# Kernel tuning notes

Hardware: AMD Instinct MI355X
Metric: run time of the kernel (lower is better)

The kernel has to match this reference:

```python
import jax, jax.numpy as jnp
import numpy as np

B, D, R, E, L = 16384, 1024, 64, 4, 2


def setup_inputs() -> dict:
    key = jax.random.key(0)
    ks = jax.random.split(key, 5)
    sU = (2.0 / (D + R)) ** 0.5  # glorot_normal std
    sC = (2.0 / (R + R)) ** 0.5
    sG = (2.0 / (D + 1)) ** 0.5
    return {
        "x": jax.random.normal(ks[0], (B, D), jnp.float32),
        "U": jax.random.normal(ks[1], (L, E, D, R), jnp.float32) * sU,
        "V": jax.random.normal(ks[2], (L, E, D, R), jnp.float32) * sU,
        "C": jax.random.normal(ks[3], (L, E, R, R), jnp.float32) * sC,
        "bias": jnp.zeros((L, D), jnp.float32),
        "gateW": jax.random.normal(ks[4], (E, D), jnp.float32) * sG,
    }


def reference(x, U, V, C, bias, gateW):
    # DCN-V2 mixture-of-low-rank-experts cross network.
    # x: [B, D]; U/V: [L, E, D, R]; C: [L, E, R, R]; bias: [L, D]; gateW: [E, D]
    x0 = x
    x_l = x
    for i in range(L):
        # gating: per-expert Dense(1, no bias) on current x_l -> softmax over experts
        gate = jax.nn.softmax(jnp.einsum('bd,ed->be', x_l, gateW), axis=-1)  # [B, E]
        # low-rank bilinear: U tanh(C tanh(V^T x)) , vectorized over experts
        v_x = jnp.tanh(jnp.einsum('edr,bd->ber', V[i], x_l))      # [B, E, R]
        c_x = jnp.tanh(jnp.einsum('erq,beq->ber', C[i], v_x))     # [B, E, R]
        uv_x = jnp.einsum('edr,ber->bed', U[i], c_x)              # [B, E, D]
        dot = x0[:, None, :] * (uv_x + bias[i][None, None, :])    # [B, E, D]
        moe_out = jnp.einsum('bed,be->bd', dot, gate)             # [B, D]
        x_l = moe_out + x_l  # residual (dropout_rate=0 -> identity)
    return x_l
```

## Files before the change

kernel.cpp:

```cpp
#include <hip/hip_runtime.h>
#include <stdint.h>


typedef __attribute__((ext_vector_type(8))) short bf16x8;
typedef __attribute__((ext_vector_type(4))) float f32x4;

#define MFMA_BF16(a, b, c) __builtin_amdgcn_mfma_f32_16x16x32_bf16((a), (b), (c), 0, 0, 0)

static constexpr int kB = 16384, kD = 1024;
static constexpr int MTILE = 32;

static constexpr size_t W1F_OFF = 0;
static constexpr size_t W1F_SZ  = 2ull * 32 * 17 * 64 * 8;
static constexpr size_t W2F_OFF = W1F_OFF + W1F_SZ;
static constexpr size_t W2F_SZ  = 2ull * 8 * 64 * 64 * 8;
static constexpr size_t CF_OFF  = W2F_OFF + W2F_SZ;

__device__ __forceinline__ unsigned short f2bf(float f) {
    uint32_t u = __builtin_bit_cast(uint32_t, f);
    u = (u + 0x7FFFu + ((u >> 16) & 1u)) >> 16;
    return (unsigned short)u;
}
__device__ __forceinline__ float bf2f(unsigned short h) {
    uint32_t u = ((uint32_t)h) << 16;
    return __builtin_bit_cast(float, u);
}
__device__ __forceinline__ float fast_tanh(float x) {
    float e = __builtin_amdgcn_exp2f(x * 2.8853900817779268f);
    return 1.0f - 2.0f * __builtin_amdgcn_rcpf(e + 1.0f);
}
__device__ __forceinline__ float fast_exp(float x) {
    return __builtin_amdgcn_exp2f(x * 1.4426950408889634f);
}

__global__ __launch_bounds__(256) void prep_weights(
    const float* __restrict__ U, const float* __restrict__ V,
    const float* __restrict__ C, const float* __restrict__ gateW,
    unsigned short* __restrict__ ws)
{
    const int id = blockIdx.x * 256 + threadIdx.x;
    const int lane = id & 63;
    const int kg = lane >> 4, c = lane & 15;
    if (id < 2 * 32 * 17 * 64) {
        int t = id >> 6;
        int nt = t % 17; t /= 17;
        int kt = t & 31; int i = t >> 5;
        int col = nt * 16 + c;
        bf16x8 o;
#pragma unroll
        for (int j = 0; j < 8; ++j) {
            int k = kt * 32 + kg * 8 + j;
            float v = 0.0f;
            if (col < 256) {
                int e = col >> 6, r = col & 63;
                v = V[((size_t)(i * 4 + e) * 1024 + k) * 64 + r];
            } else if (col < 260) {
                v = gateW[(size_t)(col - 256) * 1024 + k];
            }
            o[j] = (short)f2bf(v);
        }
        *(bf16x8*)(ws + W1F_OFF + (size_t)id * 8) = o;
    } else if (id < 2 * 32 * 17 * 64 + 2 * 8 * 64 * 64) {
        int id2 = id - 2 * 32 * 17 * 64;
        int t = id2 >> 6;
        int nt = t & 63; t >>= 6;
        int kt = t & 7;  int i = t >> 3;
        int d = nt * 16 + c;
        bf16x8 o;
#pragma unroll
        for (int j = 0; j < 8; ++j) {
            int k = kt * 32 + kg * 8 + j;
            int e = k >> 6, r = k & 63;
            o[j] = (short)f2bf(U[((size_t)(i * 4 + e) * 1024 + d) * 64 + r]);
        }
        *(bf16x8*)(ws + W2F_OFF + (size_t)id2 * 8) = o;
    } else if (id < 2 * 32 * 17 * 64 + 2 * 8 * 64 * 64 + 2 * 4 * 2 * 4 * 64) {
        int id3 = id - (2 * 32 * 17 * 64 + 2 * 8 * 64 * 64);
        int t = id3 >> 6;
        int nt = t & 3; t >>= 2;
        int kt = t & 1; t >>= 1;
        int e = t & 3;  int i = t >> 2;
        int r = nt * 16 + c;
        bf16x8 o;
#pragma unroll
        for (int j = 0; j < 8; ++j) {
            int q = kt * 32 + kg * 8 + j;
            o[j] = (short)f2bf(C[((size_t)(i * 4 + e) * 64 + r) * 64 + q]);
        }
        *(bf16x8*)(ws + CF_OFF + (size_t)id3 * 8) = o;
    }
}

__global__ __launch_bounds__(256, 2) void dcn_main(
    const float* __restrict__ x, const float* __restrict__ bias,
    const unsigned short* __restrict__ ws, float* __restrict__ out)
{
    __shared__ char smem[64 * 1024 + 16 * 1024];
    char* xl = smem;
    char* sh = smem + 64 * 1024;

    const unsigned short* w1f = ws + W1F_OFF;
    const unsigned short* w2f = ws + W2F_OFF;
    const unsigned short* cf  = ws + CF_OFF;

    const int tid = threadIdx.x;
    const int lane = tid & 63, wid = tid >> 6;
    const int kg = lane >> 4, lc = lane & 15;
    const int mbase = blockIdx.x * MTILE;

#pragma unroll
    for (int it = 0; it < 16; ++it) {
        int chunk = it * 256 + tid;
        int row = chunk >> 7, col = (chunk & 127) * 8;
        const float* src = x + (size_t)(mbase + row) * 1024 + col;
        f32x4 v0 = *(const f32x4*)src;
        f32x4 v1 = *(const f32x4*)(src + 4);
        bf16x8 hv;
        hv[0] = (short)f2bf(v0[0]); hv[1] = (short)f2bf(v0[1]);
        hv[2] = (short)f2bf(v0[2]); hv[3] = (short)f2bf(v0[3]);
        hv[4] = (short)f2bf(v1[0]); hv[5] = (short)f2bf(v1[1]);
        hv[6] = (short)f2bf(v1[2]); hv[7] = (short)f2bf(v1[3]);
        int off = (row * 2048 + col * 2) ^ ((row & 7) << 4);
        *(bf16x8*)(xl + off) = hv;
    }
    __syncthreads();

    const f32x4 zf = {0.f, 0.f, 0.f, 0.f};

    for (int i = 0; i < 2; ++i) {
        f32x4 acc1[2][4] = {{zf, zf, zf, zf}, {zf, zf, zf, zf}};
        f32x4 accg[2] = {zf, zf};
        {
            auto ldA = [&](bf16x8* a, int kt) {
#pragma unroll
                for (int mt = 0; mt < 2; ++mt) {
                    int row = mt * 16 + lc;
                    int off = (row * 2048 + (kt * 32 + kg * 8) * 2) ^ ((row & 7) << 4);
                    a[mt] = *(const bf16x8*)(xl + off);
                }
            };
            auto ldB = [&](bf16x8* b, int kt) {
                const unsigned short* wb = w1f + (size_t)(i * 32 + kt) * 17 * 512;
#pragma unroll
                for (int nt = 0; nt < 4; ++nt)
                    b[nt] = *(const bf16x8*)(wb + (wid * 4 + nt) * 512 + lane * 8);
                b[4] = *(const bf16x8*)(wb + 16 * 512 + lane * 8);
            };
            auto fm = [&](const bf16x8* a, const bf16x8* b) {
#pragma unroll
                for (int nt = 0; nt < 4; ++nt) {
                    acc1[0][nt] = MFMA_BF16(a[0], b[nt], acc1[0][nt]);
                    acc1[1][nt] = MFMA_BF16(a[1], b[nt], acc1[1][nt]);
                }
                accg[0] = MFMA_BF16(a[0], b[4], accg[0]);
                accg[1] = MFMA_BF16(a[1], b[4], accg[1]);
            };
            bf16x8 aA[2], aB[2], bA[5], bB[5];
            ldA(aA, 0); ldB(bA, 0);
#pragma unroll
            for (int k2 = 0; k2 < 16; ++k2) {
                ldA(aB, 2 * k2 + 1); ldB(bB, 2 * k2 + 1);
                fm(aA, bA);
                if (k2 < 15) { ldA(aA, 2 * k2 + 2); ldB(bA, 2 * k2 + 2); }
                fm(aB, bB);
            }
        }

        char* vsl = sh + wid * 4096;
#pragma unroll
        for (int mt = 0; mt < 2; ++mt)
#pragma unroll
        for (int nt = 0; nt < 4; ++nt)
#pragma unroll
        for (int j = 0; j < 4; ++j) {
            int row = mt * 16 + kg * 4 + j;
            int q = nt * 16 + lc;
            int off = (row * 128 + q * 2) ^ ((row & 7) << 4);
            *(unsigned short*)(vsl + off) = f2bf(fast_tanh(acc1[mt][nt][j]));
        }

        float gate_val[2][4];
#pragma unroll
        for (int mt = 0; mt < 2; ++mt)
#pragma unroll
        for (int j = 0; j < 4; ++j) {
            int base = lane & 48;
            float l0 = __shfl(accg[mt][j], base + 0);
            float l1 = __shfl(accg[mt][j], base + 1);
            float l2 = __shfl(accg[mt][j], base + 2);
            float l3 = __shfl(accg[mt][j], base + 3);
            float m = fmaxf(fmaxf(l0, l1), fmaxf(l2, l3));
            float e0 = fast_exp(l0 - m), e1 = fast_exp(l1 - m);
            float e2 = fast_exp(l2 - m), e3 = fast_exp(l3 - m);
            float ge = wid == 0 ? e0 : wid == 1 ? e1 : wid == 2 ? e2 : e3;
            gate_val[mt][j] = ge * __builtin_amdgcn_rcpf(e0 + e1 + e2 + e3);
        }

        f32x4 accc[2][4] = {{zf, zf, zf, zf}, {zf, zf, zf, zf}};
        {
            bf16x8 a0[2], a1[2], cb0[4], cb1[4];
            const unsigned short* cb = cf + (size_t)(((i * 4 + wid) * 2 + 0) * 4) * 512;
            const unsigned short* cb_1 = cf + (size_t)(((i * 4 + wid) * 2 + 1) * 4) * 512;
#pragma unroll
            for (int nt = 0; nt < 4; ++nt) {
                cb0[nt] = *(const bf16x8*)(cb + nt * 512 + lane * 8);
                cb1[nt] = *(const bf16x8*)(cb_1 + nt * 512 + lane * 8);
            }
#pragma unroll
            for (int mt = 0; mt < 2; ++mt) {
                int row = mt * 16 + lc;
                int off0 = (row * 128 + (0 * 32 + kg * 8) * 2) ^ ((row & 7) << 4);
                int off1 = (row * 128 + (1 * 32 + kg * 8) * 2) ^ ((row & 7) << 4);
                a0[mt] = *(const bf16x8*)(vsl + off0);
                a1[mt] = *(const bf16x8*)(vsl + off1);
            }
#pragma unroll
            for (int nt = 0; nt < 4; ++nt) {
                accc[0][nt] = MFMA_BF16(a0[0], cb0[nt], accc[0][nt]);
                accc[1][nt] = MFMA_BF16(a0[1], cb0[nt], accc[1][nt]);
                accc[0][nt] = MFMA_BF16(a1[0], cb1[nt], accc[0][nt]);
                accc[1][nt] = MFMA_BF16(a1[1], cb1[nt], accc[1][nt]);
            }
        }
        __syncthreads();

#pragma unroll
        for (int mt = 0; mt < 2; ++mt)
#pragma unroll
        for (int nt = 0; nt < 4; ++nt)
#pragma unroll
        for (int j = 0; j < 4; ++j) {
            int row = mt * 16 + kg * 4 + j;
            int colg = wid * 64 + nt * 16 + lc;
            float t = fast_tanh(accc[mt][nt][j]) * gate_val[mt][j];
            int off = (row * 512 + colg * 2) ^ ((row & 7) << 4);
            *(unsigned short*)(sh + off) = f2bf(t);
        }
        __syncthreads();

        for (int half = 0; half < 2; ++half) {
            f32x4 acc2[2][8];
#pragma unroll
            for (int mt = 0; mt < 2; ++mt)
#pragma unroll
            for (int nt = 0; nt < 8; ++nt) acc2[mt][nt] = zf;

            auto ldA2 = [&](bf16x8* a, int kt) {
#pragma unroll
                for (int mt = 0; mt < 2; ++mt) {
                    int row = mt * 16 + lc;
                    int off = (row * 512 + (kt * 32 + kg * 8) * 2) ^ ((row & 7) << 4);
                    a[mt] = *(const bf16x8*)(sh + off);
                }
            };
            auto ldB2 = [&](bf16x8* b, int kt) {
                const unsigned short* w2b = w2f + (size_t)(i * 8 + kt) * 64 * 512;
#pragma unroll
                for (int nt = 0; nt < 8; ++nt)
                    b[nt] = *(const bf16x8*)(w2b + (wid * 16 + half * 8 + nt) * 512 + lane * 8);
            };
            auto fm2 = [&](const bf16x8* a, const bf16x8* b) {
#pragma unroll
                for (int nt = 0; nt < 8; ++nt) {
                    acc2[0][nt] = MFMA_BF16(a[0], b[nt], acc2[0][nt]);
                    acc2[1][nt] = MFMA_BF16(a[1], b[nt], acc2[1][nt]);
                }
            };
            bf16x8 aA[2], aB[2], bA[8], bB[8];
            ldA2(aA, 0); ldB2(bA, 0);
#pragma unroll
            for (int k2 = 0; k2 < 4; ++k2) {
                ldA2(aB, 2 * k2 + 1); ldB2(bB, 2 * k2 + 1);
                fm2(aA, bA);
                if (k2 < 3) { ldA2(aA, 2 * k2 + 2); ldB2(bA, 2 * k2 + 2); }
                fm2(aB, bB);
            }

#pragma unroll
            for (int nt = 0; nt < 8; ++nt) {
                int d = wid * 256 + half * 128 + nt * 16 + lc;
                float bv = bias[(size_t)i * 1024 + d];
#pragma unroll
                for (int mt = 0; mt < 2; ++mt)
#pragma unroll
                for (int j = 0; j < 4; ++j) {
                    int row = mt * 16 + kg * 4 + j;
                    float z = acc2[mt][nt][j] + bv;
                    float x0v = x[(size_t)(mbase + row) * 1024 + d];
                    int xoff = (row * 2048 + d * 2) ^ ((row & 7) << 4);
                    float xlv = bf2f(*(const unsigned short*)(xl + xoff));
                    float o = x0v * z + xlv;
                    if (i == 0) {
                        *(unsigned short*)(xl + xoff) = f2bf(o);
                    } else {
                        out[(size_t)(mbase + row) * 1024 + d] = o;
                    }
                }
            }
        }
        __syncthreads();
    }
}

extern "C" void kernel_launch(void* const* d_in, const int* in_sizes, int n_in,
                              void* d_out, int out_size, void* d_ws, size_t ws_size,
                              hipStream_t stream) {
    const float* x     = (const float*)d_in[0];
    const float* U     = (const float*)d_in[1];
    const float* V     = (const float*)d_in[2];
    const float* C     = (const float*)d_in[3];
    const float* bias  = (const float*)d_in[4];
    const float* gateW = (const float*)d_in[5];
    unsigned short* ws = (unsigned short*)d_ws;
    float* out = (float*)d_out;

    const int prep_threads = 2 * 32 * 17 * 64 + 2 * 8 * 64 * 64 + 2 * 4 * 2 * 4 * 64;
    prep_weights<<<(prep_threads + 255) / 256, 256, 0, stream>>>(U, V, C, gateW, ws);
    dcn_main<<<kB / MTILE, 256, 0, stream>>>(x, bias, ws, out);
}
```

Before: 264.1 us.

## Split main kernel work across eight waves per block and vectorize weight prep

Doubles the workgroup to 512 threads so each expert's rank dimension is split across two waves, and halves each wave's output columns in the U projection. A barrier is added before the C stage because the V-projection tile is now written by two waves. This aims for more waves in flight to hide latency, at the cost of an extra sync and possible occupancy limits from the 80 KB LDS per block. The prep kernel's U and C conversions now use 16-byte vector loads instead of scalar loads.

```diff
diff --git a/kernel.cpp b/kernel.cpp
--- a/kernel.cpp
+++ b/kernel.cpp
@@ -66,13 +66,16 @@
         int nt = t & 63; t >>= 6;
         int kt = t & 7;  int i = t >> 3;
         int d = nt * 16 + c;
+        int k0 = kt * 32 + kg * 8;
+        int e = k0 >> 6, r0 = k0 & 63;
+        const float* src = U + ((size_t)(i * 4 + e) * 1024 + d) * 64 + r0;
+        f32x4 u0 = *(const f32x4*)src;
+        f32x4 u1 = *(const f32x4*)(src + 4);
         bf16x8 o;
-#pragma unroll
-        for (int j = 0; j < 8; ++j) {
-            int k = kt * 32 + kg * 8 + j;
-            int e = k >> 6, r = k & 63;
-            o[j] = (short)f2bf(U[((size_t)(i * 4 + e) * 1024 + d) * 64 + r]);
-        }
+        o[0] = (short)f2bf(u0[0]); o[1] = (short)f2bf(u0[1]);
+        o[2] = (short)f2bf(u0[2]); o[3] = (short)f2bf(u0[3]);
+        o[4] = (short)f2bf(u1[0]); o[5] = (short)f2bf(u1[1]);
+        o[6] = (short)f2bf(u1[2]); o[7] = (short)f2bf(u1[3]);
         *(bf16x8*)(ws + W2F_OFF + (size_t)id2 * 8) = o;
     } else if (id < 2 * 32 * 17 * 64 + 2 * 8 * 64 * 64 + 2 * 4 * 2 * 4 * 64) {
         int id3 = id - (2 * 32 * 17 * 64 + 2 * 8 * 64 * 64);
@@ -81,21 +84,24 @@
         int kt = t & 1; t >>= 1;
         int e = t & 3;  int i = t >> 2;
         int r = nt * 16 + c;
+        int q0 = kt * 32 + kg * 8;
+        const float* src = C + ((size_t)(i * 4 + e) * 64 + r) * 64 + q0;
+        f32x4 c0 = *(const f32x4*)src;
+        f32x4 c1 = *(const f32x4*)(src + 4);
         bf16x8 o;
-#pragma unroll
-        for (int j = 0; j < 8; ++j) {
-            int q = kt * 32 + kg * 8 + j;
-            o[j] = (short)f2bf(C[((size_t)(i * 4 + e) * 64 + r) * 64 + q]);
-        }
+        o[0] = (short)f2bf(c0[0]); o[1] = (short)f2bf(c0[1]);
+        o[2] = (short)f2bf(c0[2]); o[3] = (short)f2bf(c0[3]);
+        o[4] = (short)f2bf(c1[0]); o[5] = (short)f2bf(c1[1]);
+        o[6] = (short)f2bf(c1[2]); o[7] = (short)f2bf(c1[3]);
         *(bf16x8*)(ws + CF_OFF + (size_t)id3 * 8) = o;
     }
 }
 
-__global__ __launch_bounds__(256, 2) void dcn_main(
+__global__ __launch_bounds__(512, 4) void dcn_main(
     const float* __restrict__ x, const float* __restrict__ bias,
     const unsigned short* __restrict__ ws, float* __restrict__ out)
 {
-    __shared__ char smem[64 * 1024 + 16 * 1024];
+    __shared__ char smem[80 * 1024];
     char* xl = smem;
     char* sh = smem + 64 * 1024;
 
@@ -106,11 +112,12 @@
     const int tid = threadIdx.x;
     const int lane = tid & 63, wid = tid >> 6;
     const int kg = lane >> 4, lc = lane & 15;
+    const int e = wid >> 1, h = wid & 1;
     const int mbase = blockIdx.x * MTILE;
 
 #pragma unroll
-    for (int it = 0; it < 16; ++it) {
-        int chunk = it * 256 + tid;
+    for (int it = 0; it < 8; ++it) {
+        int chunk = it * 512 + tid;
         int row = chunk >> 7, col = (chunk & 127) * 8;
         const float* src = x + (size_t)(mbase + row) * 1024 + col;
         f32x4 v0 = *(const f32x4*)src;
@@ -128,7 +135,7 @@
     const f32x4 zf = {0.f, 0.f, 0.f, 0.f};
 
     for (int i = 0; i < 2; ++i) {
-        f32x4 acc1[2][4] = {{zf, zf, zf, zf}, {zf, zf, zf, zf}};
+        f32x4 acc1[2][2] = {{zf, zf}, {zf, zf}};
         f32x4 accg[2] = {zf, zf};
         {
             auto ldA = [&](bf16x8* a, int kt) {
@@ -141,21 +148,20 @@
             };
             auto ldB = [&](bf16x8* b, int kt) {
                 const unsigned short* wb = w1f + (size_t)(i * 32 + kt) * 17 * 512;
-#pragma unroll
-                for (int nt = 0; nt < 4; ++nt)
-                    b[nt] = *(const bf16x8*)(wb + (wid * 4 + nt) * 512 + lane * 8);
-                b[4] = *(const bf16x8*)(wb + 16 * 512 + lane * 8);
+                b[0] = *(const bf16x8*)(wb + (2 * wid + 0) * 512 + lane * 8);
+                b[1] = *(const bf16x8*)(wb + (2 * wid + 1) * 512 + lane * 8);
+                b[2] = *(const bf16x8*)(wb + 16 * 512 + lane * 8);
             };
             auto fm = [&](const bf16x8* a, const bf16x8* b) {
 #pragma unroll
-                for (int nt = 0; nt < 4; ++nt) {
+                for (int nt = 0; nt < 2; ++nt) {
                     acc1[0][nt] = MFMA_BF16(a[0], b[nt], acc1[0][nt]);
                     acc1[1][nt] = MFMA_BF16(a[1], b[nt], acc1[1][nt]);
                 }
-                accg[0] = MFMA_BF16(a[0], b[4], accg[0]);
-                accg[1] = MFMA_BF16(a[1], b[4], accg[1]);
-            };
-            bf16x8 aA[2], aB[2], bA[5], bB[5];
+                accg[0] = MFMA_BF16(a[0], b[2], accg[0]);
+                accg[1] = MFMA_BF16(a[1], b[2], accg[1]);
+            };
+            bf16x8 aA[2], aB[2], bA[3], bB[3];
             ldA(aA, 0); ldB(bA, 0);
 #pragma unroll
             for (int k2 = 0; k2 < 16; ++k2) {
@@ -164,19 +170,6 @@
                 if (k2 < 15) { ldA(aA, 2 * k2 + 2); ldB(bA, 2 * k2 + 2); }
                 fm(aB, bB);
             }
-        }
-
-        char* vsl = sh + wid * 4096;
-#pragma unroll
-        for (int mt = 0; mt < 2; ++mt)
-#pragma unroll
-        for (int nt = 0; nt < 4; ++nt)
-#pragma unroll
-        for (int j = 0; j < 4; ++j) {
-            int row = mt * 16 + kg * 4 + j;
-            int q = nt * 16 + lc;
-            int off = (row * 128 + q * 2) ^ ((row & 7) << 4);
-            *(unsigned short*)(vsl + off) = f2bf(fast_tanh(acc1[mt][nt][j]));
         }
 
         float gate_val[2][4];
@@ -192,19 +185,32 @@
             float m = fmaxf(fmaxf(l0, l1), fmaxf(l2, l3));
             float e0 = fast_exp(l0 - m), e1 = fast_exp(l1 - m);
             float e2 = fast_exp(l2 - m), e3 = fast_exp(l3 - m);
-            float ge = wid == 0 ? e0 : wid == 1 ? e1 : wid == 2 ? e2 : e3;
+            float ge = e == 0 ? e0 : e == 1 ? e1 : e == 2 ? e2 : e3;
             gate_val[mt][j] = ge * __builtin_amdgcn_rcpf(e0 + e1 + e2 + e3);
         }
 
-        f32x4 accc[2][4] = {{zf, zf, zf, zf}, {zf, zf, zf, zf}};
+        char* vsl = sh + e * 4096;
+#pragma unroll
+        for (int mt = 0; mt < 2; ++mt)
+#pragma unroll
+        for (int nt = 0; nt < 2; ++nt)
+#pragma unroll
+        for (int j = 0; j < 4; ++j) {
+            int row = mt * 16 + kg * 4 + j;
+            int q = h * 32 + nt * 16 + lc;
+            int off = (row * 128 + q * 2) ^ ((row & 7) << 4);
+            *(unsigned short*)(vsl + off) = f2bf(fast_tanh(acc1[mt][nt][j]));
+        }
+        __syncthreads();
+
+        f32x4 accc[2][2] = {{zf, zf}, {zf, zf}};
         {
-            bf16x8 a0[2], a1[2], cb0[4], cb1[4];
-            const unsigned short* cb = cf + (size_t)(((i * 4 + wid) * 2 + 0) * 4) * 512;
-            const unsigned short* cb_1 = cf + (size_t)(((i * 4 + wid) * 2 + 1) * 4) * 512;
-#pragma unroll
-            for (int nt = 0; nt < 4; ++nt) {
-                cb0[nt] = *(const bf16x8*)(cb + nt * 512 + lane * 8);
-                cb1[nt] = *(const bf16x8*)(cb_1 + nt * 512 + lane * 8);
+            bf16x8 a0[2], a1[2], cb0[2], cb1[2];
+            const unsigned short* cbase = cf + (size_t)((i * 4 + e) * 2) * 4 * 512;
+#pragma unroll
+            for (int nt = 0; nt < 2; ++nt) {
+                cb0[nt] = *(const bf16x8*)(cbase + (0 * 4 + h * 2 + nt) * 512 + lane * 8);
+                cb1[nt] = *(const bf16x8*)(cbase + (1 * 4 + h * 2 + nt) * 512 + lane * 8);
             }
 #pragma unroll
             for (int mt = 0; mt < 2; ++mt) {
@@ -215,7 +221,7 @@
                 a1[mt] = *(const bf16x8*)(vsl + off1);
             }
 #pragma unroll
-            for (int nt = 0; nt < 4; ++nt) {
+            for (int nt = 0; nt < 2; ++nt) {
                 accc[0][nt] = MFMA_BF16(a0[0], cb0[nt], accc[0][nt]);
                 accc[1][nt] = MFMA_BF16(a0[1], cb0[nt], accc[1][nt]);
                 accc[0][nt] = MFMA_BF16(a1[0], cb1[nt], accc[0][nt]);
@@ -227,23 +233,23 @@
 #pragma unroll
         for (int mt = 0; mt < 2; ++mt)
 #pragma unroll
-        for (int nt = 0; nt < 4; ++nt)
+        for (int nt = 0; nt < 2; ++nt)
 #pragma unroll
         for (int j = 0; j < 4; ++j) {
             int row = mt * 16 + kg * 4 + j;
-            int colg = wid * 64 + nt * 16 + lc;
+            int colg = e * 64 + h * 32 + nt * 16 + lc;
             float t = fast_tanh(accc[mt][nt][j]) * gate_val[mt][j];
             int off = (row * 512 + colg * 2) ^ ((row & 7) << 4);
             *(unsigned short*)(sh + off) = f2bf(t);
         }
         __syncthreads();
 
-        for (int half = 0; half < 2; ++half) {
-            f32x4 acc2[2][8];
+        for (int pass = 0; pass < 2; ++pass) {
+            f32x4 acc2[2][4];
 #pragma unroll
             for (int mt = 0; mt < 2; ++mt)
 #pragma unroll
-            for (int nt = 0; nt < 8; ++nt) acc2[mt][nt] = zf;
+            for (int nt = 0; nt < 4; ++nt) acc2[mt][nt] = zf;
 
             auto ldA2 = [&](bf16x8* a, int kt) {
 #pragma unroll
@@ -256,17 +262,17 @@
             auto ldB2 = [&](bf16x8* b, int kt) {
                 const unsigned short* w2b = w2f + (size_t)(i * 8 + kt) * 64 * 512;
 #pragma unroll
-                for (int nt = 0; nt < 8; ++nt)
-                    b[nt] = *(const bf16x8*)(w2b + (wid * 16 + half * 8 + nt) * 512 + lane * 8);
+                for (int nt = 0; nt < 4; ++nt)
+                    b[nt] = *(const bf16x8*)(w2b + (wid * 8 + pass * 4 + nt) * 512 + lane * 8);
             };
             auto fm2 = [&](const bf16x8* a, const bf16x8* b) {
 #pragma unroll
-                for (int nt = 0; nt < 8; ++nt) {
+                for (int nt = 0; nt < 4; ++nt) {
                     acc2[0][nt] = MFMA_BF16(a[0], b[nt], acc2[0][nt]);
                     acc2[1][nt] = MFMA_BF16(a[1], b[nt], acc2[1][nt]);
                 }
             };
-            bf16x8 aA[2], aB[2], bA[8], bB[8];
+            bf16x8 aA[2], aB[2], bA[4], bB[4];
             ldA2(aA, 0); ldB2(bA, 0);
 #pragma unroll
             for (int k2 = 0; k2 < 4; ++k2) {
@@ -277,8 +283,8 @@
             }
 
 #pragma unroll
-            for (int nt = 0; nt < 8; ++nt) {
-                int d = wid * 256 + half * 128 + nt * 16 + lc;
+            for (int nt = 0; nt < 4; ++nt) {
+                int d = wid * 128 + pass * 64 + nt * 16 + lc;
                 float bv = bias[(size_t)i * 1024 + d];
 #pragma unroll
                 for (int mt = 0; mt < 2; ++mt)
@@ -316,5 +322,5 @@
 
     const int prep_threads = 2 * 32 * 17 * 64 + 2 * 8 * 64 * 64 + 2 * 4 * 2 * 4 * 64;
     prep_weights<<<(prep_threads + 255) / 256, 256, 0, stream>>>(U, V, C, gateW, ws);
-    dcn_main<<<kB / MTILE, 256, 0, stream>>>(x, bias, ws, out);
-}
+    dcn_main<<<kB / MTILE, 512, 0, stream>>>(x, bias, ws, out);
+}
```

After: 290.0 us. 9.8% more time.
